# Kernel optimization log

Hardware: AMD Instinct MI355X
Metric: run time of the kernel (lower is better)

## Reference

```python
import jax, jax.numpy as jnp
import numpy as np

D_MODEL = 2048
EXPAND = 2
D_INNER = EXPAND * D_MODEL      # 4096
HEADDIM = 64
NHEADS = D_INNER // HEADDIM     # 64
D_STATE = 128
NGROUPS = 1
D_CONV = 4
CHUNK = 256
CONV_DIM = D_INNER + 2 * NGROUPS * D_STATE          # 4352
D_IN_PROJ = 2 * D_INNER + 2 * NGROUPS * D_STATE + NHEADS  # 8512
EPS = 1e-5


def setup_inputs() -> dict:
    key = jax.random.key(0)
    ks = jax.random.split(key, 8)
    B, L = 2, 2048
    u = jax.random.normal(ks[0], (B, L, D_MODEL), jnp.float32)
    W_in = jax.random.normal(ks[1], (D_IN_PROJ, D_MODEL), jnp.float32) / np.sqrt(D_MODEL)
    conv_w = jax.random.normal(ks[2], (CONV_DIM, D_CONV), jnp.float32) * 0.2
    conv_b = jax.random.normal(ks[3], (CONV_DIM,), jnp.float32) * 0.05
    # dt_bias initialized exactly as in the torch module
    dt = jnp.exp(jax.random.uniform(ks[4], (NHEADS,)) * (np.log(0.1) - np.log(0.001)) + np.log(0.001))
    dt = jnp.clip(dt, 1e-4)
    dt_bias = dt + jnp.log(-jnp.expm1(-dt))
    A_log = jnp.log(jax.random.uniform(ks[5], (NHEADS,), minval=1.0, maxval=16.0))
    D = jnp.ones((NHEADS,), jnp.float32)
    norm_w = jnp.ones((D_INNER,), jnp.float32)
    W_out = jax.random.normal(ks[6], (D_MODEL, D_INNER), jnp.float32) / np.sqrt(D_INNER)
    return dict(u=u, W_in=W_in, conv_w=conv_w, conv_b=conv_b, dt_bias=dt_bias,
                A_log=A_log, D=D, norm_w=norm_w, W_out=W_out)


def _segsum(x):
    # x: (..., l) -> (..., l, l) with out[i, j] = sum_{k=j+1..i} x[k] (lower-tri, -inf above)
    cs = jnp.cumsum(x, -1)
    seg = cs[..., :, None] - cs[..., None, :]
    l = x.shape[-1]
    mask = jnp.tril(jnp.ones((l, l), bool))
    return jnp.where(mask, seg, -jnp.inf)


def reference(u, W_in, conv_w, conv_b, dt_bias, A_log, D, norm_w, W_out):
    B, L, _ = u.shape
    zxbcdt = u @ W_in.T                                   # (B, L, 8512)
    z, xBC, dt_raw = jnp.split(zxbcdt, [D_INNER, D_INNER + CONV_DIM], axis=-1)
    # depthwise causal conv1d + SiLU (padding = d_conv-1, truncated to seqlen)
    xpad = jnp.pad(xBC, ((0, 0), (D_CONV - 1, 0), (0, 0)))
    xconv = conv_b + sum(xpad[:, w:w + L, :] * conv_w[:, w] for w in range(D_CONV))
    xBC = jax.nn.silu(xconv)
    x, Bm, Cm = jnp.split(xBC, [D_INNER, D_INNER + NGROUPS * D_STATE], axis=-1)
    x = x.reshape(B, L, NHEADS, HEADDIM)
    hpg = NHEADS // NGROUPS
    Bh = jnp.repeat(Bm.reshape(B, L, NGROUPS, D_STATE), hpg, axis=2)  # (B,L,H,N)
    Ch = jnp.repeat(Cm.reshape(B, L, NGROUPS, D_STATE), hpg, axis=2)
    dt = jax.nn.softplus(dt_raw + dt_bias)                # (B, L, H)
    A = -jnp.exp(A_log)                                   # (H,)
    nchunks = L // CHUNK
    def chunk(t):
        return t.reshape(B, nchunks, CHUNK, *t.shape[2:])
    xc, Bc, Cc, dtc = chunk(x), chunk(Bh), chunk(Ch), chunk(dt)
    xd = xc * dtc[..., None]                              # (B,C,Lc,H,P)
    dA = jnp.transpose(dtc * A, (0, 3, 1, 2))             # (B,H,C,Lc)
    A_cum = jnp.cumsum(dA, -1)
    Lmat = jnp.exp(_segsum(dA))                           # (B,H,C,Lc,Lc) lower-tri decays
    # intra-chunk (diagonal blocks)
    Y_diag = jnp.einsum('bclhn,bcshn,bhcls,bcshp->bclhp', Cc, Bc, Lmat, xd)
    # chunk end-states
    decay_states = jnp.exp(A_cum[..., -1:] - A_cum)       # (B,H,C,Lc)
    states = jnp.einsum('bclhn,bhcl,bclhp->bchpn', Bc, decay_states, xd)
    # inter-chunk recurrence over chunk states
    chunk_sums = jnp.pad(A_cum[..., -1], ((0, 0), (0, 0), (1, 0)))  # (B,H,C+1)
    decay_chunk = jnp.exp(_segsum(chunk_sums))            # (B,H,C+1,C+1)
    states_pad = jnp.concatenate([jnp.zeros_like(states[:, :1]), states], axis=1)
    new_states = jnp.einsum('bhzc,bchpn->bzhpn', decay_chunk, states_pad)
    prev_states = new_states[:, :-1]                      # (B,C,H,P,N)
    Y_off = jnp.einsum('bclhn,bchpn,bhcl->bclhp', Cc, prev_states, jnp.exp(A_cum))
    y = (Y_diag + Y_off).reshape(B, L, NHEADS, HEADDIM)
    y = y + x * D[None, None, :, None]                    # per-head D skip
    y = y.reshape(B, L, D_INNER)
    # gated RMSNorm (norm_before_gate=False): rmsnorm(y * silu(z)) * w
    yg = y * jax.nn.silu(z)
    var = jnp.mean(yg * yg, axis=-1, keepdims=True)
    y = yg * jax.lax.rsqrt(var + EPS) * norm_w
    return y @ W_out.T                                    # (B, L, d_model)
```

## Files before the change

### kernel.cpp

```cpp
#include <hip/hip_runtime.h>

#define D_MODEL   2048
#define D_INNER   4096
#define HEADDIM   64
#define NHEADS    64
#define D_STATE   128
#define CHUNK     256
#define CONV_DIM  4352
#define D_IN_PROJ 8512
#define BATCH     2
#define SEQ       2048
#define NCHUNK    8
#define NROWS     4096
#define EPSV      1e-5f
#define CG        (CONV_DIM / 8)

typedef __attribute__((ext_vector_type(8))) short bf16x8;
typedef __attribute__((ext_vector_type(8))) unsigned short u16x8;
typedef __attribute__((ext_vector_type(4))) float f32x4;

#define AS1 __attribute__((address_space(1)))
#define AS3 __attribute__((address_space(3)))

#define BAR() do { asm volatile("" ::: "memory"); __builtin_amdgcn_s_barrier(); asm volatile("" ::: "memory"); } while (0)

__device__ __forceinline__ unsigned short f2bf(float f) {
  unsigned int x = __float_as_uint(f);
  unsigned int r = (x + 0x7fffu + ((x >> 16) & 1u)) >> 16;
  return (unsigned short)r;
}
__device__ __forceinline__ float bf2f(unsigned short u) {
  return __uint_as_float((unsigned int)u << 16);
}

__global__ void k_sentinel(float* out) { if (threadIdx.x == 0) out[0] = 1.0e6f; }

__global__ void k_f32_to_bf16_v4(const float* __restrict__ in, unsigned short* __restrict__ out, long n4) {
  long i = (long)blockIdx.x * blockDim.x + threadIdx.x;
  long stride = (long)gridDim.x * blockDim.x;
  for (; i < n4; i += stride) {
    float4 v = ((const float4*)in)[i];
    ushort4 o = make_ushort4(f2bf(v.x), f2bf(v.y), f2bf(v.z), f2bf(v.w));
    ((ushort4*)out)[i] = o;
  }
}

__global__ void k_usplit(const float* __restrict__ in, unsigned short* __restrict__ hi,
                         unsigned short* __restrict__ lo, long n4) {
  long i = (long)blockIdx.x * blockDim.x + threadIdx.x;
  long stride = (long)gridDim.x * blockDim.x;
  for (; i < n4; i += stride) {
    float4 v = ((const float4*)in)[i];
    ushort4 h, l;
    h.x = f2bf(v.x); l.x = f2bf(v.x - bf2f(h.x));
    h.y = f2bf(v.y); l.y = f2bf(v.y - bf2f(h.y));
    h.z = f2bf(v.z); l.z = f2bf(v.z - bf2f(h.z));
    h.w = f2bf(v.w); l.w = f2bf(v.w - bf2f(h.w));
    ((ushort4*)hi)[i] = h;
    ((ushort4*)lo)[i] = l;
  }
}

__global__ void k_wpack(const float* __restrict__ W, unsigned short* __restrict__ whl) {
  long i = (long)blockIdx.x * blockDim.x + threadIdx.x;
  if (i >= (long)64 * D_MODEL) return;
  float v = W[(size_t)8448 * D_MODEL + i];
  unsigned short h = f2bf(v);
  whl[i] = h;
  whl[(size_t)64 * D_MODEL + i] = f2bf(v - bf2f(h));
}

__global__ __launch_bounds__(256, 2) void k_dtm(const unsigned short* __restrict__ uhi,
                                                const unsigned short* __restrict__ ulo,
                                                const unsigned short* __restrict__ whl,
                                                const float* __restrict__ dt_bias,
                                                float* __restrict__ dt_t) {
  __shared__ __align__(16) short lds[2][256 * 64];
  const int t = threadIdx.x;
  const int lane = t & 63;
  const int w = t >> 6;
  const int m0 = (int)blockIdx.x * 64;

  f32x4 acc1[8], acc2[4];
#pragma unroll
  for (int j = 0; j < 8; ++j) { f32x4 z = {0.f, 0.f, 0.f, 0.f}; acc1[j] = z; }
#pragma unroll
  for (int j = 0; j < 4; ++j) { f32x4 z = {0.f, 0.f, 0.f, 0.f}; acc2[j] = z; }

  const int srow = t >> 3;
  const int schunk = (t & 7) ^ (srow & 7);
  const unsigned short* gU = uhi + (size_t)(m0 + srow) * D_MODEL + schunk * 8;
  const unsigned short* gL = ulo + (size_t)(m0 + srow) * D_MODEL + schunk * 8;
  const unsigned short* gW = whl + (size_t)srow * D_MODEL + schunk * 8;

  auto STAGE = [&](int buf, int kt) {
    char* d = (char*)&lds[buf][0] + t * 16;
#pragma unroll
    for (int ii = 0; ii < 2; ++ii)
      __builtin_amdgcn_global_load_lds((const AS1 void*)(gU + (size_t)ii * 32 * D_MODEL + (size_t)kt * 64),
                                       (AS3 void*)(d + ii * 4096), 16, 0, 0);
#pragma unroll
    for (int ii = 0; ii < 2; ++ii)
      __builtin_amdgcn_global_load_lds((const AS1 void*)(gL + (size_t)ii * 32 * D_MODEL + (size_t)kt * 64),
                                       (AS3 void*)(d + 8192 + ii * 4096), 16, 0, 0);
#pragma unroll
    for (int ii = 0; ii < 4; ++ii)
      __builtin_amdgcn_global_load_lds((const AS1 void*)(gW + (size_t)ii * 32 * D_MODEL + (size_t)kt * 64),
                                       (AS3 void*)(d + 16384 + ii * 4096), 16, 0, 0);
  };

  STAGE(0, 0);

  const int NT = D_MODEL / 64;
  const int ar = w * 16 + (lane & 15);
  const int kof = (lane >> 4) * 8;
  const int rsw = (lane & 7) * 8;
  int cur = 0;
  for (int kt = 0; kt < NT; ++kt) {
    if (kt + 1 < NT) {
      STAGE(cur ^ 1, kt + 1);
      asm volatile("s_waitcnt vmcnt(8)" ::: "memory");
    } else {
      asm volatile("s_waitcnt vmcnt(0)" ::: "memory");
    }
    __builtin_amdgcn_s_barrier();
    asm volatile("" ::: "memory");
    const short* L = &lds[cur][0];
#pragma unroll
    for (int kk = 0; kk < 2; ++kk) {
      const int off = (kk * 32 + kof) ^ rsw;
      bf16x8 ah = *(const bf16x8*)(L + ar * 64 + off);
      bf16x8 al = *(const bf16x8*)(L + (64 + ar) * 64 + off);
#pragma unroll
      for (int j = 0; j < 8; ++j) {
        bf16x8 bj = *(const bf16x8*)(L + (128 + j * 16 + (lane & 15)) * 64 + off);
        acc1[j] = __builtin_amdgcn_mfma_f32_16x16x32_bf16(ah, bj, acc1[j], 0, 0, 0);
        if (j < 4) acc2[j] = __builtin_amdgcn_mfma_f32_16x16x32_bf16(al, bj, acc2[j], 0, 0, 0);
      }
    }
    asm volatile("" ::: "memory");
    __builtin_amdgcn_s_barrier();
    asm volatile("" ::: "memory");
    cur ^= 1;
  }

  const int crow = (lane >> 4) * 4;
#pragma unroll
  for (int j = 0; j < 4; ++j) {
    int h = j * 16 + (lane & 15);
    float bias = dt_bias[h];
#pragma unroll
    for (int r = 0; r < 4; ++r) {
      int row = m0 + w * 16 + crow + r;
      float v = acc1[j][r] + acc1[j + 4][r] + acc2[j][r] + bias;
      float dtv = (v > 20.f) ? v : log1pf(expf(v));
      dt_t[(size_t)((row >> 11) * NHEADS + h) * SEQ + (row & 2047)] = dtv;
    }
  }
}

__global__ __launch_bounds__(512, 2) void k_gemm8p(const unsigned short* __restrict__ A,
                                                   const unsigned short* __restrict__ B,
                                                   unsigned short* __restrict__ C, int M, int N, int K) {
  __shared__ __align__(16) short lds[2][32768];
  const int t = threadIdx.x;
  const int lane = t & 63;
  const int wid = t >> 6;
  const int wr = wid >> 2;
  const int wc = wid & 3;
  const int ntx = N / 256;
  const int nwg = (int)gridDim.x;
  const int bid = (int)blockIdx.x;
  const int swzb = (bid & 7) * (nwg >> 3) + (bid >> 3);
  const int m0 = (swzb / ntx) * 256;
  const int n0 = (swzb % ntx) * 256;

  f32x4 acc[8][4];
#pragma unroll
  for (int i = 0; i < 8; ++i)
#pragma unroll
    for (int j = 0; j < 4; ++j) { f32x4 z = {0.f, 0.f, 0.f, 0.f}; acc[i][j] = z; }

  const int srow = t >> 3;
  const int schunk = (t & 7) ^ (srow & 7);
  const unsigned short* gA = A + (size_t)(m0 + srow) * K + schunk * 8;
  const unsigned short* gB = B + (size_t)(n0 + srow) * K + schunk * 8;

  auto STAGE_HALF = [&](int buf, int kt, int which) {
    const unsigned short* g = (which < 2 ? gA : gB) + (size_t)(which & 1) * 128 * K + (size_t)kt * 64;
    char* d = (char*)lds + buf * 65536 + which * 16384 + t * 16;
    __builtin_amdgcn_global_load_lds((const AS1 void*)g, (AS3 void*)d, 16, 0, 0);
    __builtin_amdgcn_global_load_lds((const AS1 void*)(g + (size_t)64 * K), (AS3 void*)(d + 8192), 16, 0, 0);
  };

  const int NT = K / 64;
  STAGE_HALF(0, 0, 0); STAGE_HALF(0, 0, 1); STAGE_HALF(0, 0, 2); STAGE_HALF(0, 0, 3);
  STAGE_HALF(1, 1, 2); STAGE_HALF(1, 1, 0); STAGE_HALF(1, 1, 1);
  asm volatile("s_waitcnt vmcnt(6)" ::: "memory");
  BAR();

  const int ar = wr * 128 + (lane & 15);
  const int br = wc * 64 + (lane & 15);
  const int kof = (lane >> 4) * 8;
  const int rsw = (lane & 7) * 8;

  for (int kt = 0; kt < NT; ++kt) {
    const int buf = kt & 1;
    const short* As = &lds[buf][0];
    const short* Bs = &lds[buf][16384];
    const bool s1 = (kt + 1 < NT);
    const bool s2 = (kt + 2 < NT);
    bf16x8 aLo[4][2], aHi[4][2], bLo[2][2], bHi[2][2];

#pragma unroll
    for (int i = 0; i < 4; ++i)
#pragma unroll
      for (int k = 0; k < 2; ++k) aLo[i][k] = *(const bf16x8*)(As + (ar + i * 16) * 64 + ((k * 32 + kof) ^ rsw));
#pragma unroll
    for (int j = 0; j < 2; ++j)
#pragma unroll
      for (int k = 0; k < 2; ++k) bLo[j][k] = *(const bf16x8*)(Bs + (br + j * 16) * 64 + ((k * 32 + kof) ^ rsw));
    if (s1) STAGE_HALF(buf ^ 1, kt + 1, 3);
    BAR();
    __builtin_amdgcn_s_setprio(1);
#pragma unroll
    for (int k = 0; k < 2; ++k)
#pragma unroll
      for (int i = 0; i < 4; ++i)
#pragma unroll
        for (int j = 0; j < 2; ++j)
          acc[i][j] = __builtin_amdgcn_mfma_f32_16x16x32_bf16(aLo[i][k], bLo[j][k], acc[i][j], 0, 0, 0);
    __builtin_amdgcn_s_setprio(0);
    BAR();

#pragma unroll
    for (int j = 0; j < 2; ++j)
#pragma unroll
      for (int k = 0; k < 2; ++k) bHi[j][k] = *(const bf16x8*)(Bs + (br + (j + 2) * 16) * 64 + ((k * 32 + kof) ^ rsw));
    BAR();
    __builtin_amdgcn_s_setprio(1);
#pragma unroll
    for (int k = 0; k < 2; ++k)
#pragma unroll
      for (int i = 0; i < 4; ++i)
#pragma unroll
        for (int j = 0; j < 2; ++j)
          acc[i][j + 2] = __builtin_amdgcn_mfma_f32_16x16x32_bf16(aLo[i][k], bHi[j][k], acc[i][j + 2], 0, 0, 0);
    __builtin_amdgcn_s_setprio(0);
    BAR();

#pragma unroll
    for (int i = 0; i < 4; ++i)
#pragma unroll
      for (int k = 0; k < 2; ++k) aHi[i][k] = *(const bf16x8*)(As + (ar + (i + 4) * 16) * 64 + ((k * 32 + kof) ^ rsw));
    if (s2) STAGE_HALF(buf, kt + 2, 2);
    BAR();
    __builtin_amdgcn_s_setprio(1);
#pragma unroll
    for (int k = 0; k < 2; ++k)
#pragma unroll
      for (int i = 0; i < 4; ++i)
#pragma unroll
        for (int j = 0; j < 2; ++j)
          acc[i + 4][j] = __builtin_amdgcn_mfma_f32_16x16x32_bf16(aHi[i][k], bLo[j][k], acc[i + 4][j], 0, 0, 0);
    __builtin_amdgcn_s_setprio(0);
    BAR();

    if (s2) { STAGE_HALF(buf, kt + 2, 0); STAGE_HALF(buf, kt + 2, 1); }
    if (s2) { asm volatile("s_waitcnt vmcnt(6)" ::: "memory"); }
    else    { asm volatile("s_waitcnt vmcnt(0)" ::: "memory"); }
    BAR();
    __builtin_amdgcn_s_setprio(1);
#pragma unroll
    for (int k = 0; k < 2; ++k)
#pragma unroll
      for (int i = 0; i < 4; ++i)
#pragma unroll
        for (int j = 0; j < 2; ++j)
          acc[i + 4][j + 2] = __builtin_amdgcn_mfma_f32_16x16x32_bf16(aHi[i][k], bHi[j][k], acc[i + 4][j + 2], 0, 0, 0);
    __builtin_amdgcn_s_setprio(0);
    BAR();
  }

  const int crow = (lane >> 4) * 4;
  const int ccol = lane & 15;
#pragma unroll
  for (int i = 0; i < 8; ++i)
#pragma unroll
    for (int j = 0; j < 4; ++j) {
      size_t base = (size_t)(m0 + wr * 128 + i * 16 + crow) * N + (n0 + wc * 64 + j * 16 + ccol);
#pragma unroll
      for (int r = 0; r < 4; ++r) C[base + (size_t)r * N] = f2bf(acc[i][j][r]);
    }
}

template <int BF16OUT>
__global__ __launch_bounds__(256, 2) void k_gemm128(const unsigned short* __restrict__ A,
                                                    const unsigned short* __restrict__ B,
                                                    void* __restrict__ Cv, int M, int N, int K) {
  constexpr int BK = 64;
  __shared__ __align__(16) short lds[2][256 * BK];
  const int t = threadIdx.x;
  const int lane = t & 63;
  const int wid = t >> 6;
  const int wr = wid >> 1;
  const int wc = wid & 1;
  const int ntx = N / 128;
  const int nwg = (int)gridDim.x;
  const int bid = (int)blockIdx.x;
  const int swzb = (bid & 7) * (nwg >> 3) + (bid >> 3);
  const int m0 = (swzb / ntx) * 128;
  const int n0 = (swzb % ntx) * 128;

  f32x4 acc[4][4];
#pragma unroll
  for (int i = 0; i < 4; ++i)
#pragma unroll
    for (int j = 0; j < 4; ++j) { f32x4 z = {0.f, 0.f, 0.f, 0.f}; acc[i][j] = z; }

  const int srow = t >> 3;
  const int schunk = (t & 7) ^ (srow & 7);
  const unsigned short* gA = A + (size_t)(m0 + srow) * K + schunk * 8;
  const unsigned short* gB = B + (size_t)(n0 + srow) * K + schunk * 8;

  auto STAGE = [&](int buf, int kt) {
    char* dA = (char*)&lds[buf][0] + t * 16;
    char* dB = (char*)&lds[buf][128 * BK] + t * 16;
#pragma unroll
    for (int ii = 0; ii < 4; ++ii)
      __builtin_amdgcn_global_load_lds((const AS1 void*)(gA + (size_t)ii * 32 * K + kt * BK),
                                       (AS3 void*)(dA + ii * 4096), 16, 0, 0);
#pragma unroll
    for (int ii = 0; ii < 4; ++ii)
      __builtin_amdgcn_global_load_lds((const AS1 void*)(gB + (size_t)ii * 32 * K + kt * BK),
                                       (AS3 void*)(dB + ii * 4096), 16, 0, 0);
  };

  STAGE(0, 0);

  const int NT = K / BK;
  const int ar = wr * 64 + (lane & 15);
  const int br = wc * 64 + (lane & 15);
  const int kof = (lane >> 4) * 8;
  const int rsw = (lane & 7) * 8;
  int cur = 0;
  for (int kt = 0; kt < NT; ++kt) {
    if (kt + 1 < NT) {
      STAGE(cur ^ 1, kt + 1);
      asm volatile("s_waitcnt vmcnt(8)" ::: "memory");
    } else {
      asm volatile("s_waitcnt vmcnt(0)" ::: "memory");
    }
    __builtin_amdgcn_s_barrier();
    asm volatile("" ::: "memory");
    const short* As = &lds[cur][0];
    const short* Bs = &lds[cur][128 * BK];
#pragma unroll
    for (int kk = 0; kk < 2; ++kk) {
      bf16x8 bfr[4];
#pragma unroll
      for (int j = 0; j < 4; ++j)
        bfr[j] = *(const bf16x8*)(Bs + (br + j * 16) * BK + ((kk * 32 + kof) ^ rsw));
#pragma unroll
      for (int i = 0; i < 4; ++i) {
        bf16x8 af = *(const bf16x8*)(As + (ar + i * 16) * BK + ((kk * 32 + kof) ^ rsw));
#pragma unroll
        for (int j = 0; j < 4; ++j)
          acc[i][j] = __builtin_amdgcn_mfma_f32_16x16x32_bf16(af, bfr[j], acc[i][j], 0, 0, 0);
      }
    }
    asm volatile("" ::: "memory");
    __builtin_amdgcn_s_barrier();
    asm volatile("" ::: "memory");
    cur ^= 1;
  }

  const int crow = (lane >> 4) * 4;
  const int ccol = lane & 15;
#pragma unroll
  for (int i = 0; i < 4; ++i)
#pragma unroll
    for (int j = 0; j < 4; ++j) {
      size_t base = (size_t)(m0 + wr * 64 + i * 16 + crow) * N + (n0 + wc * 64 + j * 16 + ccol);
      if (BF16OUT) {
        unsigned short* C = (unsigned short*)Cv;
#pragma unroll
        for (int r = 0; r < 4; ++r) C[base + (size_t)r * N] = f2bf(acc[i][j][r]);
      } else {
        float* C = (float*)Cv;
#pragma unroll
        for (int r = 0; r < 4; ++r) C[base + (size_t)r * N] = acc[i][j][r];
      }
    }
}

__global__ void k_conv_pack(const float* __restrict__ cw, const float* __restrict__ cb,
                            unsigned short* __restrict__ wT, unsigned short* __restrict__ bT) {
  int i = blockIdx.x * blockDim.x + threadIdx.x;
  if (i < CONV_DIM) {
#pragma unroll
    for (int w = 0; w < 4; ++w) wT[w * CONV_DIM + i] = f2bf(cw[i * 4 + w]);
    bT[i] = f2bf(cb[i]);
  }
}

__global__ __launch_bounds__(256) void k_conv_silu(const unsigned short* __restrict__ xb,
                                                   const unsigned short* __restrict__ wT,
                                                   const unsigned short* __restrict__ bT,
                                                   unsigned short* __restrict__ out) {
  long idx = (long)blockIdx.x * blockDim.x + threadIdx.x;
  if (idx >= (long)(NROWS / 4) * CG) return;
  int c8 = (int)(idx % CG);
  long rq = idx / CG;
  int l0 = (int)((rq & (SEQ / 4 - 1)) * 4);
  long brow = (rq >> 9) * (long)SEQ;
  int ch0 = c8 * 8;

  u16x8 wv[4];
#pragma unroll
  for (int w = 0; w < 4; ++w) wv[w] = *(const u16x8*)(wT + w * CONV_DIM + ch0);
  u16x8 bv = *(const u16x8*)(bT + ch0);

  u16x8 xr[7];
#pragma unroll
  for (int i = 0; i < 7; ++i) {
    int ls = l0 - 3 + i;
    if (ls >= 0) xr[i] = *(const u16x8*)(xb + (brow + ls) * (long)CONV_DIM + ch0);
    else { u16x8 z = {0, 0, 0, 0, 0, 0, 0, 0}; xr[i] = z; }
  }

#pragma unroll
  for (int r = 0; r < 4; ++r) {
    float acc[8];
#pragma unroll
    for (int e = 0; e < 8; ++e) acc[e] = bf2f(bv[e]);
#pragma unroll
    for (int w = 0; w < 4; ++w)
#pragma unroll
      for (int e = 0; e < 8; ++e) acc[e] += bf2f(xr[r + w][e]) * bf2f(wv[w][e]);
    u16x8 o;
#pragma unroll
    for (int e = 0; e < 8; ++e) o[e] = f2bf(acc[e] / (1.f + expf(-acc[e])));
    *(u16x8*)(out + (brow + l0 + r) * (long)CONV_DIM + ch0) = o;
  }
}

__global__ __launch_bounds__(256) void k_cumsum(const float* __restrict__ dt_t, const float* __restrict__ A_log,
                                                float* __restrict__ A_cum) {
  const int bid = blockIdx.x;
  const int c = bid & 7;
  const int bh = bid >> 3;
  const int h = bh & 63;
  const int l = threadIdx.x;
  float A = -expf(A_log[h]);
  __shared__ float s[256];
  s[l] = dt_t[(size_t)bh * SEQ + c * CHUNK + l] * A;
  __syncthreads();
  for (int off = 1; off < 256; off <<= 1) {
    float x = (l >= off) ? s[l - off] : 0.f;
    __syncthreads();
    s[l] += x;
    __syncthreads();
  }
  A_cum[(size_t)bid * CHUNK + l] = s[l];
}

__global__ __launch_bounds__(256) void k_cbtt(const unsigned short* __restrict__ xbc, unsigned short* __restrict__ cbt_t) {
  const int bid = blockIdx.x;
  const int sp = bid & 3;
  const int bc = bid >> 2;
  const int b = bc >> 3, c = bc & 7;
  const int t = threadIdx.x;
  const int lane = t & 63;
  const int w = t >> 6;
  const int g = lane >> 4;
  __shared__ unsigned short Cs[256][72];
  __shared__ unsigned short Bs2[64][72];
  const long rowbase = (long)b * SEQ + c * CHUNK;
  f32x4 acc[4][4];
#pragma unroll
  for (int i = 0; i < 4; ++i)
#pragma unroll
    for (int j = 0; j < 4; ++j) { f32x4 z = {0.f, 0.f, 0.f, 0.f}; acc[i][j] = z; }

  for (int np = 0; np < 2; ++np) {
    __syncthreads();
    for (int i = t; i < 256 * 16; i += 256) {
      int row = i >> 4, c4 = (i & 15) * 4;
      ushort4 v = *(const ushort4*)(xbc + (rowbase + row) * (long)CONV_DIM + D_INNER + D_STATE + np * 64 + c4);
      *(ushort4*)&Cs[row][c4] = v;
    }
    for (int i = t; i < 64 * 16; i += 256) {
      int row = i >> 4, c4 = (i & 15) * 4;
      ushort4 v = *(const ushort4*)(xbc + (rowbase + sp * 64 + row) * (long)CONV_DIM + D_INNER + np * 64 + c4);
      *(ushort4*)&Bs2[row][c4] = v;
    }
    __syncthreads();
#pragma unroll
    for (int ks = 0; ks < 2; ++ks) {
      const int kofs = ks * 32 + g * 8;
      bf16x8 af[4], bfr[4];
#pragma unroll
      for (int i = 0; i < 4; ++i) af[i] = *(const bf16x8*)&Cs[w * 64 + i * 16 + (lane & 15)][kofs];
#pragma unroll
      for (int j = 0; j < 4; ++j) bfr[j] = *(const bf16x8*)&Bs2[j * 16 + (lane & 15)][kofs];
#pragma unroll
      for (int i = 0; i < 4; ++i)
#pragma unroll
        for (int j = 0; j < 4; ++j)
          acc[i][j] = __builtin_amdgcn_mfma_f32_16x16x32_bf16(af[i], bfr[j], acc[i][j], 0, 0, 0);
    }
  }
  unsigned short* ob = cbt_t + (long)bc * CHUNK * CHUNK;
#pragma unroll
  for (int i = 0; i < 4; ++i)
#pragma unroll
    for (int j = 0; j < 4; ++j) {
      int l0 = w * 64 + i * 16 + g * 4;
      int s = sp * 64 + j * 16 + (lane & 15);
#pragma unroll
      for (int r = 0; r < 4; ++r) ob[(long)(l0 + r) * CHUNK + s] = f2bf(acc[i][j][r]);
    }
}

__global__ __launch_bounds__(256) void k_states(const unsigned short* __restrict__ xbc, const float* __restrict__ dt_t,
                                                const float* __restrict__ A_cum, float* __restrict__ states) {
  const int bid = blockIdx.x;
  const int h = bid & 63;
  const int bc = bid >> 6;
  const int b = bc >> 3, c = bc & 7;
  const int t = threadIdx.x;
  const int lane = t & 63;
  const int w = t >> 6;
  const int g = lane >> 4;
  __shared__ unsigned short BT[128][72];
  __shared__ unsigned short WXT[64][72];
  __shared__ float csL[256], dtL[256];
  const long rowbase = (long)b * SEQ + c * CHUNK;
  const long bh8 = ((long)(b * NHEADS + h)) * NCHUNK + c;
  const float* acum = A_cum + bh8 * CHUNK;
  if (t < 256) { csL[t] = acum[t]; dtL[t] = dt_t[((size_t)(b * NHEADS + h)) * SEQ + c * CHUNK + t]; }
  float cs_last = acum[255];
  f32x4 acc[2][4];
#pragma unroll
  for (int i = 0; i < 2; ++i)
#pragma unroll
    for (int j = 0; j < 4; ++j) { f32x4 z = {0.f, 0.f, 0.f, 0.f}; acc[i][j] = z; }

  for (int lp = 0; lp < 4; ++lp) {
    __syncthreads();
    for (int i = t; i < 64 * 32; i += 256) {
      int l = i >> 5, n4 = (i & 31) * 4;
      ushort4 v = *(const ushort4*)(xbc + (rowbase + lp * 64 + l) * (long)CONV_DIM + D_INNER + n4);
      BT[n4 + 0][l] = v.x; BT[n4 + 1][l] = v.y; BT[n4 + 2][l] = v.z; BT[n4 + 3][l] = v.w;
    }
    for (int i = t; i < 64 * 16; i += 256) {
      int l = i >> 4, p4 = (i & 15) * 4;
      int lg = lp * 64 + l;
      float wgt = expf(cs_last - csL[lg]) * dtL[lg];
      ushort4 v = *(const ushort4*)(xbc + (rowbase + lg) * (long)CONV_DIM + h * HEADDIM + p4);
      WXT[p4 + 0][l] = f2bf(bf2f(v.x) * wgt);
      WXT[p4 + 1][l] = f2bf(bf2f(v.y) * wgt);
      WXT[p4 + 2][l] = f2bf(bf2f(v.z) * wgt);
      WXT[p4 + 3][l] = f2bf(bf2f(v.w) * wgt);
    }
    __syncthreads();
#pragma unroll
    for (int ks = 0; ks < 2; ++ks) {
      const int kofs = ks * 32 + g * 8;
      bf16x8 am[2], bp[4];
#pragma unroll
      for (int i = 0; i < 2; ++i) am[i] = *(const bf16x8*)&BT[w * 32 + i * 16 + (lane & 15)][kofs];
#pragma unroll
      for (int j = 0; j < 4; ++j) bp[j] = *(const bf16x8*)&WXT[j * 16 + (lane & 15)][kofs];
#pragma unroll
      for (int i = 0; i < 2; ++i)
#pragma unroll
        for (int j = 0; j < 4; ++j)
          acc[i][j] = __builtin_amdgcn_mfma_f32_16x16x32_bf16(am[i], bp[j], acc[i][j], 0, 0, 0);
    }
  }
  float* sp = states + ((long)bc * NHEADS + h) * (D_STATE * HEADDIM);
#pragma unroll
  for (int i = 0; i < 2; ++i)
#pragma unroll
    for (int j = 0; j < 4; ++j) {
      int n0 = w * 32 + i * 16 + g * 4;
      int p = j * 16 + (lane & 15);
#pragma unroll
      for (int r = 0; r < 4; ++r) sp[(long)(n0 + r) * HEADDIM + p] = acc[i][j][r];
    }
}

__global__ void k_scan(const float* __restrict__ states, const float* __restrict__ A_cum, unsigned short* __restrict__ psb) {
  long idx = (long)blockIdx.x * blockDim.x + threadIdx.x;
  if (idx >= (long)BATCH * NHEADS * D_STATE * HEADDIM) return;
  int p = idx & 63;
  int n = (int)((idx >> 6) & 127);
  long bh = idx >> 13;
  int h = (int)(bh & 63);
  int b = (int)(bh >> 6);
  float S = 0.f;
  for (int c = 0; c < NCHUNK; ++c) {
    long soff = (((long)(b * NCHUNK + c) * NHEADS + h) * (D_STATE * HEADDIM)) + (long)n * HEADDIM + p;
    psb[soff] = f2bf(S);
    float decay = expf(A_cum[(bh * NCHUNK + c) * CHUNK + 255]);
    S = S * decay + states[soff];
  }
}

__global__ __launch_bounds__(256) void k_y(const unsigned short* __restrict__ xbc, const float* __restrict__ dt_t,
                                           const float* __restrict__ A_cum, const unsigned short* __restrict__ cbt_t,
                                           const unsigned short* __restrict__ psb, const float* __restrict__ Dp,
                                           unsigned short* __restrict__ y) {
  const int bid = blockIdx.x;
  const int h = bid & 63;
  const int bc = bid >> 6;
  const int b = bc >> 3, c = bc & 7;
  const int t = threadIdx.x;
  const int lane = t & 63;
  const int w = t >> 6;
  const int g = lane >> 4;
  __shared__ unsigned short Abuf[256][72];
  __shared__ unsigned short Bbuf[64][72];
  __shared__ float csL[256], dtL[256], expL[256];
  const long rowbase = (long)b * SEQ + c * CHUNK;
  const long bh8 = ((long)(b * NHEADS + h)) * NCHUNK + c;
  const float* acum = A_cum + bh8 * CHUNK;
  if (t < 256) {
    float cv = acum[t];
    csL[t] = cv;
    expL[t] = expf(cv);
    dtL[t] = dt_t[((size_t)(b * NHEADS + h)) * SEQ + c * CHUNK + t];
  }
  f32x4 acc[4][4];
#pragma unroll
  for (int i = 0; i < 4; ++i)
#pragma unroll
    for (int j = 0; j < 4; ++j) { f32x4 z = {0.f, 0.f, 0.f, 0.f}; acc[i][j] = z; }

  const unsigned short* psbase = psb + ((long)bc * NHEADS + h) * (D_STATE * HEADDIM);
  for (int np = 0; np < 2; ++np) {
    __syncthreads();
    for (int i = t; i < 256 * 16; i += 256) {
      int row = i >> 4, c4 = (i & 15) * 4;
      float el = expL[row];
      ushort4 v = *(const ushort4*)(xbc + (rowbase + row) * (long)CONV_DIM + D_INNER + D_STATE + np * 64 + c4);
      ushort4 o = make_ushort4(f2bf(bf2f(v.x) * el), f2bf(bf2f(v.y) * el), f2bf(bf2f(v.z) * el), f2bf(bf2f(v.w) * el));
      *(ushort4*)&Abuf[row][c4] = o;
    }
    for (int i = t; i < 64 * 16; i += 256) {
      int n = i >> 4, p4 = (i & 15) * 4;
      ushort4 v = *(const ushort4*)(psbase + (long)(np * 64 + n) * HEADDIM + p4);
      Bbuf[p4 + 0][n] = v.x; Bbuf[p4 + 1][n] = v.y; Bbuf[p4 + 2][n] = v.z; Bbuf[p4 + 3][n] = v.w;
    }
    __syncthreads();
#pragma unroll
    for (int ks = 0; ks < 2; ++ks) {
      const int kofs = ks * 32 + g * 8;
      bf16x8 af[4], bfr[4];
#pragma unroll
      for (int i = 0; i < 4; ++i) af[i] = *(const bf16x8*)&Abuf[w * 64 + i * 16 + (lane & 15)][kofs];
#pragma unroll
      for (int j = 0; j < 4; ++j) bfr[j] = *(const bf16x8*)&Bbuf[j * 16 + (lane & 15)][kofs];
#pragma unroll
      for (int i = 0; i < 4; ++i)
#pragma unroll
        for (int j = 0; j < 4; ++j)
          acc[i][j] = __builtin_amdgcn_mfma_f32_16x16x32_bf16(af[i], bfr[j], acc[i][j], 0, 0, 0);
    }
  }

  const unsigned short* cbtb = cbt_t + (long)bc * CHUNK * CHUNK;
  for (int sp = 0; sp < 4; ++sp) {
    __syncthreads();
    for (int i = t; i < 64 * 8; i += 256) {
      int s = i >> 3, p0 = (i & 7) * 8;
      u16x8 v = *(const u16x8*)(xbc + (rowbase + sp * 64 + s) * (long)CONV_DIM + h * HEADDIM + p0);
#pragma unroll
      for (int e = 0; e < 8; ++e) Bbuf[p0 + e][s] = v[e];
    }
    __syncthreads();
    if (sp > w) continue;
#pragma unroll
    for (int ks = 0; ks < 2; ++ks) {
      const int kofs = ks * 32 + g * 8;
      bf16x8 bfr[4];
#pragma unroll
      for (int j = 0; j < 4; ++j) bfr[j] = *(const bf16x8*)&Bbuf[j * 16 + (lane & 15)][kofs];
      const int sbase = sp * 64 + ks * 32 + g * 8;
#pragma unroll
      for (int i = 0; i < 4; ++i) {
        if (sp == w && ks * 32 > i * 16 + 15) continue;
        const int l = w * 64 + i * 16 + (lane & 15);
        u16x8 cv = *(const u16x8*)(cbtb + (long)l * CHUNK + sbase);
        const float cl = csL[l];
        bf16x8 af;
#pragma unroll
        for (int e = 0; e < 8; ++e) {
          int s = sbase + e;
          float val = (s <= l) ? bf2f(cv[e]) * expf(cl - csL[s]) * dtL[s] : 0.f;
          af[e] = (short)f2bf(val);
        }
#pragma unroll
        for (int j = 0; j < 4; ++j)
          acc[i][j] = __builtin_amdgcn_mfma_f32_16x16x32_bf16(af, bfr[j], acc[i][j], 0, 0, 0);
      }
    }
  }

  const float Dh = Dp[h];
#pragma unroll
  for (int i = 0; i < 4; ++i) {
    int l0 = w * 64 + i * 16 + g * 4;
#pragma unroll
    for (int r = 0; r < 4; ++r) {
      long grow = rowbase + l0 + r;
      const unsigned short* xrow = xbc + grow * (long)CONV_DIM + h * HEADDIM;
      unsigned short* yrow = y + grow * (long)D_INNER + h * HEADDIM;
#pragma unroll
      for (int j = 0; j < 4; ++j) {
        int p = j * 16 + (lane & 15);
        yrow[p] = f2bf(acc[i][j][r] + bf2f(xrow[p]) * Dh);
      }
    }
  }
}

__global__ __launch_bounds__(256) void k_norm(unsigned short* yz, const unsigned short* __restrict__ zb,
                                              const float* __restrict__ norm_w, unsigned short* out) {
  const int row = blockIdx.x;
  const int t = threadIdx.x;
  const unsigned short* yr = yz + (size_t)row * D_INNER;
  const unsigned short* zr = zb + (size_t)row * D_INNER;
  float yv[16];
  float ss = 0.f;
#pragma unroll
  for (int j = 0; j < 4; ++j) {
    int e = (t + j * 256) * 4;
    ushort4 yy = *(const ushort4*)(yr + e);
    ushort4 zz = *(const ushort4*)(zr + e);
    float z0 = bf2f(zz.x), z1 = bf2f(zz.y), z2 = bf2f(zz.z), z3 = bf2f(zz.w);
    float g0 = bf2f(yy.x) * z0 / (1.f + expf(-z0));
    float g1 = bf2f(yy.y) * z1 / (1.f + expf(-z1));
    float g2 = bf2f(yy.z) * z2 / (1.f + expf(-z2));
    float g3 = bf2f(yy.w) * z3 / (1.f + expf(-z3));
    ss += g0 * g0 + g1 * g1 + g2 * g2 + g3 * g3;
    yv[j * 4 + 0] = g0; yv[j * 4 + 1] = g1; yv[j * 4 + 2] = g2; yv[j * 4 + 3] = g3;
  }
#pragma unroll
  for (int off = 32; off > 0; off >>= 1) ss += __shfl_xor(ss, off);
  __shared__ float red[4];
  if ((t & 63) == 0) red[t >> 6] = ss;
  __syncthreads();
  float tot = red[0] + red[1] + red[2] + red[3];
  float scale = rsqrtf(tot / (float)D_INNER + EPSV);
  unsigned short* orow = out + (size_t)row * D_INNER;
#pragma unroll
  for (int j = 0; j < 4; ++j) {
    int e = (t + j * 256) * 4;
    float4 w = *(const float4*)(norm_w + e);
    ushort4 o = make_ushort4(f2bf(yv[j * 4 + 0] * scale * w.x), f2bf(yv[j * 4 + 1] * scale * w.y),
                             f2bf(yv[j * 4 + 2] * scale * w.z), f2bf(yv[j * 4 + 3] * scale * w.w));
    *(ushort4*)(orow + e) = o;
  }
}

extern "C" void kernel_launch(void* const* d_in, const int* in_sizes, int n_in,
                              void* d_out, int out_size, void* d_ws, size_t ws_size,
                              hipStream_t stream) {
  const float* u       = (const float*)d_in[0];
  const float* W_in    = (const float*)d_in[1];
  const float* conv_w  = (const float*)d_in[2];
  const float* conv_b  = (const float*)d_in[3];
  const float* dt_bias = (const float*)d_in[4];
  const float* A_log   = (const float*)d_in[5];
  const float* Dp      = (const float*)d_in[6];
  const float* norm_w  = (const float*)d_in[7];
  const float* W_out   = (const float*)d_in[8];
  float* out = (float*)d_out;

  char* ws = (char*)d_ws;
  size_t off = 0;
  auto alloc = [&](size_t bytes) { char* p = ws + off; off += (bytes + 255) & ~(size_t)255; return p; };
  unsigned short* ub   = (unsigned short*)alloc((size_t)NROWS * D_MODEL * 2);
  unsigned short* winb = (unsigned short*)alloc((size_t)D_IN_PROJ * D_MODEL * 2);
  unsigned short* zb   = (unsigned short*)alloc((size_t)NROWS * D_INNER * 2);
  unsigned short* xb   = (unsigned short*)alloc((size_t)NROWS * CONV_DIM * 2);
  unsigned short* xbcb = (unsigned short*)alloc((size_t)NROWS * CONV_DIM * 2);
  float* dtt  = (float*)alloc((size_t)BATCH * NHEADS * SEQ * 4);
  float* acum = (float*)alloc((size_t)BATCH * NHEADS * NCHUNK * CHUNK * 4);
  unsigned short* cwT = (unsigned short*)alloc((size_t)4 * CONV_DIM * 2);
  unsigned short* cbT = (unsigned short*)alloc((size_t)CONV_DIM * 2);
  unsigned short* whl = (unsigned short*)alloc((size_t)128 * D_MODEL * 2);
  unsigned short* wob = ub;
  unsigned short* cbt = winb;
  unsigned short* psb = winb + (size_t)BATCH * NCHUNK * CHUNK * CHUNK + 1024;
  unsigned short* ulob = xbcb;
  unsigned short* yb = xb;
  float* states = (float*)d_out;

  if (off > ws_size) {
    k_sentinel<<<1, 64, 0, stream>>>(out);
    return;
  }

  k_usplit<<<2048, 256, 0, stream>>>(u, ub, ulob, (long)NROWS * D_MODEL / 4);
  k_f32_to_bf16_v4<<<2048, 256, 0, stream>>>(W_in, winb, (long)D_IN_PROJ * D_MODEL / 4);
  k_wpack<<<(64 * D_MODEL + 255) / 256, 256, 0, stream>>>(W_in, whl);
  k_conv_pack<<<(CONV_DIM + 255) / 256, 256, 0, stream>>>(conv_w, conv_b, cwT, cbT);
  k_gemm8p<<<(NROWS / 256) * (D_INNER / 256), 512, 0, stream>>>(ub, winb, zb, NROWS, D_INNER, D_MODEL);
  k_gemm128<1><<<(NROWS / 128) * (CONV_DIM / 128), 256, 0, stream>>>(ub, winb + (size_t)D_INNER * D_MODEL, xb, NROWS, CONV_DIM, D_MODEL);
  k_dtm<<<NROWS / 64, 256, 0, stream>>>(ub, ulob, whl, dt_bias, dtt);
  k_conv_silu<<<(int)(((long)(NROWS / 4) * CG + 255) / 256), 256, 0, stream>>>(xb, cwT, cbT, xbcb);
  k_cumsum<<<BATCH * NHEADS * NCHUNK, 256, 0, stream>>>(dtt, A_log, acum);
  k_cbtt<<<BATCH * NCHUNK * 4, 256, 0, stream>>>(xbcb, cbt);
  k_states<<<BATCH * NCHUNK * NHEADS, 256, 0, stream>>>(xbcb, dtt, acum, states);
  k_scan<<<(BATCH * NHEADS * D_STATE * HEADDIM + 255) / 256, 256, 0, stream>>>(states, acum, psb);
  k_y<<<BATCH * NCHUNK * NHEADS, 256, 0, stream>>>(xbcb, dtt, acum, cbt, psb, Dp, yb);
  k_norm<<<NROWS, 256, 0, stream>>>(yb, zb, norm_w, yb);
  k_f32_to_bf16_v4<<<2048, 256, 0, stream>>>(W_out, wob, (long)D_MODEL * D_INNER / 4);
  k_gemm128<0><<<(NROWS / 128) * (D_MODEL / 128), 256, 0, stream>>>(yb, wob, out, NROWS, D_MODEL, D_INNER);
}
```

Before: 507.0 us.

## Split-K the dt projection GEMM and fuse reduction with softplus and cumsum

```diff
diff --git a/kernel.cpp b/kernel.cpp
--- a/kernel.cpp
+++ b/kernel.cpp
@@ -73,13 +73,14 @@
 __global__ __launch_bounds__(256, 2) void k_dtm(const unsigned short* __restrict__ uhi,
                                                 const unsigned short* __restrict__ ulo,
                                                 const unsigned short* __restrict__ whl,
-                                                const float* __restrict__ dt_bias,
-                                                float* __restrict__ dt_t) {
+                                                float* __restrict__ PD) {
   __shared__ __align__(16) short lds[2][256 * 64];
   const int t = threadIdx.x;
   const int lane = t & 63;
   const int w = t >> 6;
-  const int m0 = (int)blockIdx.x * 64;
+  const int ks = (int)blockIdx.x & 3;
+  const int m0 = ((int)blockIdx.x >> 2) * 64;
+  const int kbase = ks * 512;
 
   f32x4 acc1[8], acc2[4];
 #pragma unroll
@@ -89,9 +90,9 @@
 
   const int srow = t >> 3;
   const int schunk = (t & 7) ^ (srow & 7);
-  const unsigned short* gU = uhi + (size_t)(m0 + srow) * D_MODEL + schunk * 8;
-  const unsigned short* gL = ulo + (size_t)(m0 + srow) * D_MODEL + schunk * 8;
-  const unsigned short* gW = whl + (size_t)srow * D_MODEL + schunk * 8;
+  const unsigned short* gU = uhi + (size_t)(m0 + srow) * D_MODEL + kbase + schunk * 8;
+  const unsigned short* gL = ulo + (size_t)(m0 + srow) * D_MODEL + kbase + schunk * 8;
+  const unsigned short* gW = whl + (size_t)srow * D_MODEL + kbase + schunk * 8;
 
   auto STAGE = [&](int buf, int kt) {
     char* d = (char*)&lds[buf][0] + t * 16;
@@ -111,7 +112,7 @@
 
   STAGE(0, 0);
 
-  const int NT = D_MODEL / 64;
+  const int NT = 512 / 64;
   const int ar = w * 16 + (lane & 15);
   const int kof = (lane >> 4) * 8;
   const int rsw = (lane & 7) * 8;
@@ -145,17 +146,45 @@
   }
 
   const int crow = (lane >> 4) * 4;
+  float* P = PD + (size_t)ks * BATCH * NHEADS * SEQ;
 #pragma unroll
   for (int j = 0; j < 4; ++j) {
     int h = j * 16 + (lane & 15);
-    float bias = dt_bias[h];
 #pragma unroll
     for (int r = 0; r < 4; ++r) {
       int row = m0 + w * 16 + crow + r;
-      float v = acc1[j][r] + acc1[j + 4][r] + acc2[j][r] + bias;
-      float dtv = (v > 20.f) ? v : log1pf(expf(v));
-      dt_t[(size_t)((row >> 11) * NHEADS + h) * SEQ + (row & 2047)] = dtv;
-    }
+      float v = acc1[j][r] + acc1[j + 4][r] + acc2[j][r];
+      P[(size_t)((row >> 11) * NHEADS + h) * SEQ + (row & 2047)] = v;
+    }
+  }
+}
+
+__global__ __launch_bounds__(256) void k_dtred(const float* __restrict__ PD, const float* __restrict__ dt_bias,
+                                               const float* __restrict__ A_log,
+                                               float* __restrict__ dt_t, float* __restrict__ A_cum) {
+  const int bh = blockIdx.x;
+  const int h = bh & 63;
+  const int t = threadIdx.x;
+  const float bias = dt_bias[h];
+  const float A = -expf(A_log[h]);
+  const size_t base = (size_t)bh * SEQ;
+  const size_t pstride = (size_t)BATCH * NHEADS * SEQ;
+  __shared__ float s[256];
+  for (int c = 0; c < NCHUNK; ++c) {
+    int l = c * CHUNK + t;
+    float v = PD[base + l] + PD[pstride + base + l] + PD[2 * pstride + base + l] + PD[3 * pstride + base + l] + bias;
+    float dtv = (v > 20.f) ? v : log1pf(expf(v));
+    dt_t[base + l] = dtv;
+    s[t] = dtv * A;
+    __syncthreads();
+    for (int off = 1; off < 256; off <<= 1) {
+      float x = (t >= off) ? s[t - off] : 0.f;
+      __syncthreads();
+      s[t] += x;
+      __syncthreads();
+    }
+    A_cum[((size_t)bh * NCHUNK + c) * CHUNK + t] = s[t];
+    __syncthreads();
   }
 }
 
@@ -443,26 +472,6 @@
     for (int e = 0; e < 8; ++e) o[e] = f2bf(acc[e] / (1.f + expf(-acc[e])));
     *(u16x8*)(out + (brow + l0 + r) * (long)CONV_DIM + ch0) = o;
   }
-}
-
-__global__ __launch_bounds__(256) void k_cumsum(const float* __restrict__ dt_t, const float* __restrict__ A_log,
-                                                float* __restrict__ A_cum) {
-  const int bid = blockIdx.x;
-  const int c = bid & 7;
-  const int bh = bid >> 3;
-  const int h = bh & 63;
-  const int l = threadIdx.x;
-  float A = -expf(A_log[h]);
-  __shared__ float s[256];
-  s[l] = dt_t[(size_t)bh * SEQ + c * CHUNK + l] * A;
-  __syncthreads();
-  for (int off = 1; off < 256; off <<= 1) {
-    float x = (l >= off) ? s[l - off] : 0.f;
-    __syncthreads();
-    s[l] += x;
-    __syncthreads();
-  }
-  A_cum[(size_t)bid * CHUNK + l] = s[l];
 }
 
 __global__ __launch_bounds__(256) void k_cbtt(const unsigned short* __restrict__ xbc, unsigned short* __restrict__ cbt_t) {
@@ -793,6 +802,7 @@
   unsigned short* cwT = (unsigned short*)alloc((size_t)4 * CONV_DIM * 2);
   unsigned short* cbT = (unsigned short*)alloc((size_t)CONV_DIM * 2);
   unsigned short* whl = (unsigned short*)alloc((size_t)128 * D_MODEL * 2);
+  float* PD = (float*)alloc((size_t)4 * BATCH * NHEADS * SEQ * 4);
   unsigned short* wob = ub;
   unsigned short* cbt = winb;
   unsigned short* psb = winb + (size_t)BATCH * NCHUNK * CHUNK * CHUNK + 1024;
@@ -811,9 +821,9 @@
   k_conv_pack<<<(CONV_DIM + 255) / 256, 256, 0, stream>>>(conv_w, conv_b, cwT, cbT);
   k_gemm8p<<<(NROWS / 256) * (D_INNER / 256), 512, 0, stream>>>(ub, winb, zb, NROWS, D_INNER, D_MODEL);
   k_gemm128<1><<<(NROWS / 128) * (CONV_DIM / 128), 256, 0, stream>>>(ub, winb + (size_t)D_INNER * D_MODEL, xb, NROWS, CONV_DIM, D_MODEL);
-  k_dtm<<<NROWS / 64, 256, 0, stream>>>(ub, ulob, whl, dt_bias, dtt);
+  k_dtm<<<256, 256, 0, stream>>>(ub, ulob, whl, PD);
+  k_dtred<<<BATCH * NHEADS, 256, 0, stream>>>(PD, dt_bias, A_log, dtt, acum);
   k_conv_silu<<<(int)(((long)(NROWS / 4) * CG + 255) / 256), 256, 0, stream>>>(xb, cwT, cbT, xbcb);
-  k_cumsum<<<BATCH * NHEADS * NCHUNK, 256, 0, stream>>>(dtt, A_log, acum);
   k_cbtt<<<BATCH * NCHUNK * 4, 256, 0, stream>>>(xbcb, cbt);
   k_states<<<BATCH * NCHUNK * NHEADS, 256, 0, stream>>>(xbcb, dtt, acum, states);
   k_scan<<<(BATCH * NHEADS * D_STATE * HEADDIM + 255) / 256, 256, 0, stream>>>(states, acum, psb);
```

Result: no change. 499.9 us (-1.4%).
